# Optimization experiments

Measured on AMD Instinct MI355X. Metric: run time of the kernel, lower is better.

## Reference

```python
import jax, jax.numpy as jnp
import numpy as np

INIT_DIM = 512
HID = 1024
OUT = 64
N_NODES = 100000
N_NBR = 65536


def setup_inputs() -> dict:
    key = jax.random.key(0)
    ks = jax.random.split(key, 12)
    inp = {}
    inp["feat"] = jax.random.normal(ks[0], (1, INIT_DIM), dtype=jnp.float32)
    for i, t in enumerate("abc"):
        inp[f"all_feat_{t}"] = jax.random.normal(ks[1 + i], (N_NODES, INIT_DIM), dtype=jnp.float32)
        inp[f"nbr_{t}"] = jax.random.randint(ks[4 + i], (N_NBR,), 0, N_NODES)
        inp[f"W1_{t}"] = jax.random.normal(ks[7 + i], (HID, INIT_DIM), dtype=jnp.float32) * 0.02
        inp[f"b1_{t}"] = jnp.zeros((HID,), dtype=jnp.float32)
    inp["Wc"] = jax.random.normal(ks[10], (OUT, HID), dtype=jnp.float32) * 0.02
    inp["bc"] = jnp.zeros((OUT,), dtype=jnp.float32)
    return inp


def reference(feat, all_feat_a, all_feat_b, all_feat_c,
              nbr_a, nbr_b, nbr_c,
              W1_a, b1_a, W1_b, b1_b, W1_c, b1_c, Wc, bc):
    # trans1 = 'rel-linear': per-type neighbor gather + relation-specific Linear
    # h_j: [N_NBR, HID]
    h_a = all_feat_a[nbr_a] @ W1_a.T + b1_a
    h_b = all_feat_b[nbr_b] @ W1_b.T + b1_b
    h_c = all_feat_c[nbr_c] @ W1_c.T + b1_c
    # trans2 = 'none' (passthrough); concat aggregation over all types
    h = jnp.concatenate([h_a, h_b, h_c], axis=0)  # [3*N_NBR, HID]
    h = jax.nn.relu(h)                             # activate = 'relu'
    pooled = h.mean(axis=0)                        # agg_node = 'mean' -> [HID]
    feat_all = jax.nn.relu(pooled)
    logits = feat_all @ Wc.T + bc                  # [OUT]
    return logits
```

## Files before the change

### kernel.cpp

```cpp
#include <hip/hip_runtime.h>
#include <hip/hip_bf16.h>

typedef __attribute__((ext_vector_type(4))) float f32x4;
typedef __attribute__((ext_vector_type(4))) int   int4v;
typedef __attribute__((ext_vector_type(2))) int   int2v;
typedef __attribute__((ext_vector_type(16))) int  i32x16;

#define N_NBR 65536
#define INIT_DIM 512
#define HID 1024
#define NPAIR 1536
#define NBLOCK 256
#define PPB 6
#define SA 24.0f
#define SW 1024.0f
#define INVS (1.0f / (24.0f * 1024.0f))

static __device__ __forceinline__ int q8(float x, float s) {
  float y = fminf(fmaxf(x * s, -127.f), 127.f);
  return __float2int_rn(y);
}
static __device__ __forceinline__ int pack4(float a, float b, float c, float d, float s) {
  return (q8(a,s) & 255) | ((q8(b,s) & 255) << 8) | ((q8(c,s) & 255) << 16) | ((q8(d,s) & 255) << 24);
}

__global__ __launch_bounds__(256) void k_convw(const float* __restrict__ wa,
                                               const float* __restrict__ wb,
                                               const float* __restrict__ wc,
                                               char* __restrict__ out) {
  int g = blockIdx.x * 256 + threadIdx.x;
  int l = g & 63;
  int blk = g >> 6;
  int ks = blk & 15;
  int nb = (blk >> 4) & 31;
  int t = blk >> 9;
  const float* src = (t == 0) ? wa : (t == 1) ? wb : wc;
  int n = nb * 32 + (l & 31);
  int k0 = ks * 32 + (l >> 5) * 16;
  const f32x4* p = (const f32x4*)(src + (size_t)n * INIT_DIM + k0);
  f32x4 x0 = p[0], x1 = p[1], x2 = p[2], x3 = p[3];
  int4v v;
  v[0] = pack4(x0.x, x0.y, x0.z, x0.w, SW);
  v[1] = pack4(x1.x, x1.y, x1.z, x1.w, SW);
  v[2] = pack4(x2.x, x2.y, x2.z, x2.w, SW);
  v[3] = pack4(x3.x, x3.y, x3.z, x3.w, SW);
  *(int4v*)(out + (size_t)g * 16) = v;
}

__global__ __launch_bounds__(512, 2) void k_main(
    const float* __restrict__ fa, const float* __restrict__ fb, const float* __restrict__ fc,
    const int* __restrict__ na, const int* __restrict__ nb_, const int* __restrict__ nc__,
    const float* __restrict__ b1a, const float* __restrict__ b1b, const float* __restrict__ b1c,
    const char* __restrict__ wbf8,
    float* __restrict__ partials) {
  __shared__ __align__(16) char Asm[64 * 1024];

  int bx = blockIdx.x;
  int tid = threadIdx.x;
  int wave = tid >> 6;
  int lane = tid & 63;
  int l31 = lane & 31, hi = lane >> 5;

  unsigned swz = (unsigned)l31 << 4;
  unsigned abase = (unsigned)l31 * 1024u + (((unsigned)hi << 4) ^ (swz & 16u));
  unsigned swzhi = swz & 0x1E0u;

  for (int jp = 0; jp < PPB; ++jp) {
    int pair = bx * PPB + jp;
    int t = pair >> 9;
    int mt0 = (pair & 511) * 2;
    const float* feat = (t == 0) ? fa : (t == 1) ? fb : fc;
    const int*   nbr  = (t == 0) ? na : (t == 1) ? nb_ : nc__;
    const float* bias = (t == 0) ? b1a : (t == 1) ? b1b : b1c;
    const char*  Wf8  = wbf8 + (size_t)t * (32 * 16 * 1024);

    if (jp) __syncthreads();

    #pragma unroll
    for (int tl = 0; tl < 2; ++tl) {
      #pragma unroll 4
      for (int c = 0; c < 8; ++c) {
        int r = c * 8 + wave;
        int idx = nbr[(mt0 + tl) * 64 + r];
        const float* rp = feat + (size_t)idx * INIT_DIM + lane * 8;
        f32x4 a  = __builtin_nontemporal_load((const f32x4*)rp);
        f32x4 b2 = __builtin_nontemporal_load((const f32x4*)rp + 1);
        int2v v;
        v[0] = pack4(a.x, a.y, a.z, a.w, SA);
        v[1] = pack4(b2.x, b2.y, b2.z, b2.w, SA);
        unsigned byte = (unsigned)r * 1024u + (unsigned)(tl * 512) +
                        (((unsigned)lane * 8u) ^ ((unsigned)(r & 31) << 4));
        *(int2v*)(Asm + byte) = v;
      }
    }
    __syncthreads();

    #pragma unroll
    for (int p = 0; p < 2; ++p) {
      const char* pBa = Wf8 + ((size_t)(wave * 4 + p * 2)     << 14) + lane * 16;
      const char* pBb = Wf8 + ((size_t)(wave * 4 + p * 2 + 1) << 14) + lane * 16;

      i32x16 acc[2][2][2] = {};
      #pragma unroll 4
      for (int ks = 0; ks < 16; ++ks) {
        int4v Bf0 = *(const int4v*)(pBa + (ks << 10));
        int4v Bf1 = *(const int4v*)(pBb + (ks << 10));
        unsigned kcol = (((unsigned)ks << 5) ^ swzhi);
        int4v Af[2][2];
        #pragma unroll
        for (int tl = 0; tl < 2; ++tl)
          #pragma unroll
          for (int i = 0; i < 2; ++i)
            Af[tl][i] = *(const int4v*)(Asm + (abase + (unsigned)(tl * 512) +
                                               (unsigned)(i * 32768) + kcol));
        #pragma unroll
        for (int tl = 0; tl < 2; ++tl)
          #pragma unroll
          for (int i = 0; i < 2; ++i) {
            acc[tl][i][0] = __builtin_amdgcn_mfma_i32_32x32x32_i8(Af[tl][i], Bf0, acc[tl][i][0], 0, 0, 0);
            acc[tl][i][1] = __builtin_amdgcn_mfma_i32_32x32x32_i8(Af[tl][i], Bf1, acc[tl][i][1], 0, 0, 0);
          }
      }

      #pragma unroll
      for (int j = 0; j < 2; ++j) {
        int n = (wave * 4 + p * 2 + j) * 32 + l31;
        float b = bias[n];
        float s = 0.f;
        #pragma unroll
        for (int tl = 0; tl < 2; ++tl)
          #pragma unroll
          for (int i = 0; i < 2; ++i)
            #pragma unroll
            for (int r = 0; r < 16; ++r) {
              float v = (float)acc[tl][i][j][r] * INVS + b;
              s += fmaxf(v, 0.f);
            }
        s += __shfl_xor(s, 32);
        if (hi == 0) partials[(size_t)pair * HID + n] = s;
      }
    }
  }
}

__global__ __launch_bounds__(256) void k_reduce(const float* __restrict__ partials,
                                                float* __restrict__ acc) {
  __shared__ float red[4][64];
  int tid = threadIdx.x;
  int c = tid & 63, rg = tid >> 6;
  int col = blockIdx.x * 64 + c;
  float s = 0.f;
  #pragma unroll 4
  for (int r = rg; r < NPAIR; r += 4)
    s += partials[(size_t)r * HID + col];
  red[rg][c] = s;
  __syncthreads();
  if (rg == 0) acc[col] = red[0][c] + red[1][c] + red[2][c] + red[3][c];
}

__global__ __launch_bounds__(256) void k_final(const float* __restrict__ acc,
                                               const float* __restrict__ Wc,
                                               const float* __restrict__ bc,
                                               float* __restrict__ out) {
  __shared__ float fall[HID];
  int tid = threadIdx.x;
  const float inv = 1.f / (3.f * (float)N_NBR);
  for (int i = tid; i < HID; i += 256) {
    float p = acc[i] * inv;
    fall[i] = (p > 0.f) ? p : 0.f;
  }
  __syncthreads();
  int o = tid >> 2, q = tid & 3;
  const f32x4* w = (const f32x4*)(Wc + (size_t)o * HID + q * 256);
  const f32x4* f = (const f32x4*)(fall + q * 256);
  float s = 0.f;
  #pragma unroll 4
  for (int k = 0; k < 64; ++k) {
    f32x4 wv = w[k], fv = f[k];
    s += wv.x * fv.x + wv.y * fv.y + wv.z * fv.z + wv.w * fv.w;
  }
  s += __shfl_xor(s, 1);
  s += __shfl_xor(s, 2);
  if (q == 0) out[o] = s + bc[o];
}

extern "C" void kernel_launch(void* const* d_in, const int* in_sizes, int n_in,
                              void* d_out, int out_size, void* d_ws, size_t ws_size,
                              hipStream_t stream) {
  const float* fa  = (const float*)d_in[1];
  const int*   na  = (const int*)d_in[2];
  const float* W1a = (const float*)d_in[3];
  const float* b1a = (const float*)d_in[4];
  const float* fb  = (const float*)d_in[5];
  const int*   nb  = (const int*)d_in[6];
  const float* W1b = (const float*)d_in[7];
  const float* b1b = (const float*)d_in[8];
  const float* fc  = (const float*)d_in[9];
  const int*   nc  = (const int*)d_in[10];
  const float* W1c = (const float*)d_in[11];
  const float* b1c = (const float*)d_in[12];
  const float* Wc  = (const float*)d_in[13];
  const float* bc  = (const float*)d_in[14];
  float* out = (float*)d_out;

  float* acc = (float*)d_ws;
  char*  wbf8 = (char*)d_ws + 4096;
  float* partials = (float*)((char*)d_ws + 4096 + 3 * 32 * 16 * 1024);

  k_convw<<<384, 256, 0, stream>>>(W1a, W1b, W1c, wbf8);
  k_main<<<NBLOCK, 512, 0, stream>>>(fa, fb, fc, na, nb, nc, b1a, b1b, b1c, wbf8, partials);
  k_reduce<<<16, 256, 0, stream>>>(partials, acc);
  k_final<<<1, 256, 0, stream>>>(acc, Wc, bc, out);
}
```

Before: 212.0 us.

## Launch one 64-row tile per block and do bias+ReLU in integer domain

The persistent 256-block kernel that looped over six 128-row pairs is replaced by 3072 independent 256-thread blocks, each gathering and quantizing a single 64-row tile into 32KB of LDS. This removes the intra-block serialization between gather and MFMA phases and lets more blocks co-reside so gathers overlap with compute across blocks. The epilogue now quantizes the bias into the int32 accumulator scale and does ReLU and summation in integers, converting to float once. In exchange each block rereads its type's full weight matrix for only 64 rows, doubling weight traffic from L2, and the partials buffer and reduction grow to twice as many rows.

```diff
diff --git a/kernel.cpp b/kernel.cpp
--- a/kernel.cpp
+++ b/kernel.cpp
@@ -9,9 +9,7 @@
 #define N_NBR 65536
 #define INIT_DIM 512
 #define HID 1024
-#define NPAIR 1536
-#define NBLOCK 256
-#define PPB 6
+#define NTILE 3072
 #define SA 24.0f
 #define SW 1024.0f
 #define INVS (1.0f / (24.0f * 1024.0f))
@@ -47,98 +45,81 @@
   *(int4v*)(out + (size_t)g * 16) = v;
 }
 
-__global__ __launch_bounds__(512, 2) void k_main(
+__global__ __launch_bounds__(256) void k_main(
     const float* __restrict__ fa, const float* __restrict__ fb, const float* __restrict__ fc,
     const int* __restrict__ na, const int* __restrict__ nb_, const int* __restrict__ nc__,
     const float* __restrict__ b1a, const float* __restrict__ b1b, const float* __restrict__ b1c,
     const char* __restrict__ wbf8,
     float* __restrict__ partials) {
-  __shared__ __align__(16) char Asm[64 * 1024];
+  __shared__ __align__(16) char Asm[64 * 512];
 
   int bx = blockIdx.x;
+  int t = bx >> 10;
+  int mtile = bx & 1023;
+  const float* feat = (t == 0) ? fa : (t == 1) ? fb : fc;
+  const int*   nbr  = (t == 0) ? na : (t == 1) ? nb_ : nc__;
+  const float* bias = (t == 0) ? b1a : (t == 1) ? b1b : b1c;
+  const char*  Wf8  = wbf8 + (size_t)t * (32 * 16 * 1024);
+
   int tid = threadIdx.x;
   int wave = tid >> 6;
   int lane = tid & 63;
   int l31 = lane & 31, hi = lane >> 5;
 
+  #pragma unroll 4
+  for (int c = 0; c < 16; ++c) {
+    int r = c * 4 + wave;
+    int idx = nbr[mtile * 64 + r];
+    const float* rp = feat + (size_t)idx * INIT_DIM + lane * 8;
+    f32x4 a  = __builtin_nontemporal_load((const f32x4*)rp);
+    f32x4 b2 = __builtin_nontemporal_load((const f32x4*)rp + 1);
+    int2v v;
+    v[0] = pack4(a.x, a.y, a.z, a.w, SA);
+    v[1] = pack4(b2.x, b2.y, b2.z, b2.w, SA);
+    unsigned byte = (unsigned)r * 512u +
+                    (((unsigned)lane * 8u) ^ ((unsigned)(r & 31) << 4));
+    *(int2v*)(Asm + byte) = v;
+  }
+  __syncthreads();
+
   unsigned swz = (unsigned)l31 << 4;
-  unsigned abase = (unsigned)l31 * 1024u + (((unsigned)hi << 4) ^ (swz & 16u));
+  unsigned abase = (unsigned)l31 * 512u + (((unsigned)hi << 4) ^ (swz & 16u));
   unsigned swzhi = swz & 0x1E0u;
 
-  for (int jp = 0; jp < PPB; ++jp) {
-    int pair = bx * PPB + jp;
-    int t = pair >> 9;
-    int mt0 = (pair & 511) * 2;
-    const float* feat = (t == 0) ? fa : (t == 1) ? fb : fc;
-    const int*   nbr  = (t == 0) ? na : (t == 1) ? nb_ : nc__;
-    const float* bias = (t == 0) ? b1a : (t == 1) ? b1b : b1c;
-    const char*  Wf8  = wbf8 + (size_t)t * (32 * 16 * 1024);
+  #pragma unroll
+  for (int p = 0; p < 4; ++p) {
+    const char* pBa = Wf8 + ((size_t)(wave * 8 + p * 2)     << 14) + lane * 16;
+    const char* pBb = Wf8 + ((size_t)(wave * 8 + p * 2 + 1) << 14) + lane * 16;
 
-    if (jp) __syncthreads();
+    i32x16 acc[2][2] = {};
+    #pragma unroll 4
+    for (int ks = 0; ks < 16; ++ks) {
+      int4v Bf0 = *(const int4v*)(pBa + (ks << 10));
+      int4v Bf1 = *(const int4v*)(pBb + (ks << 10));
+      unsigned kcol = (((unsigned)ks << 5) ^ swzhi);
+      int4v Af[2];
+      #pragma unroll
+      for (int i = 0; i < 2; ++i)
+        Af[i] = *(const int4v*)(Asm + (abase + (unsigned)(i * 16384) + kcol));
+      #pragma unroll
+      for (int i = 0; i < 2; ++i) {
+        acc[i][0] = __builtin_amdgcn_mfma_i32_32x32x32_i8(Af[i], Bf0, acc[i][0], 0, 0, 0);
+        acc[i][1] = __builtin_amdgcn_mfma_i32_32x32x32_i8(Af[i], Bf1, acc[i][1], 0, 0, 0);
+      }
+    }
 
     #pragma unroll
-    for (int tl = 0; tl < 2; ++tl) {
-      #pragma unroll 4
-      for (int c = 0; c < 8; ++c) {
-        int r = c * 8 + wave;
-        int idx = nbr[(mt0 + tl) * 64 + r];
-        const float* rp = feat + (size_t)idx * INIT_DIM + lane * 8;
-        f32x4 a  = __builtin_nontemporal_load((const f32x4*)rp);
-        f32x4 b2 = __builtin_nontemporal_load((const f32x4*)rp + 1);
-        int2v v;
-        v[0] = pack4(a.x, a.y, a.z, a.w, SA);
-        v[1] = pack4(b2.x, b2.y, b2.z, b2.w, SA);
-        unsigned byte = (unsigned)r * 1024u + (unsigned)(tl * 512) +
-                        (((unsigned)lane * 8u) ^ ((unsigned)(r & 31) << 4));
-        *(int2v*)(Asm + byte) = v;
-      }
-    }
-    __syncthreads();
-
-    #pragma unroll
-    for (int p = 0; p < 2; ++p) {
-      const char* pBa = Wf8 + ((size_t)(wave * 4 + p * 2)     << 14) + lane * 16;
-      const char* pBb = Wf8 + ((size_t)(wave * 4 + p * 2 + 1) << 14) + lane * 16;
-
-      i32x16 acc[2][2][2] = {};
-      #pragma unroll 4
-      for (int ks = 0; ks < 16; ++ks) {
-        int4v Bf0 = *(const int4v*)(pBa + (ks << 10));
-        int4v Bf1 = *(const int4v*)(pBb + (ks << 10));
-        unsigned kcol = (((unsigned)ks << 5) ^ swzhi);
-        int4v Af[2][2];
+    for (int j = 0; j < 2; ++j) {
+      int n = (wave * 8 + p * 2 + j) * 32 + l31;
+      int bq = __float2int_rn(bias[n] * (SA * SW));
+      int s = 0;
+      #pragma unroll
+      for (int i = 0; i < 2; ++i)
         #pragma unroll
-        for (int tl = 0; tl < 2; ++tl)
-          #pragma unroll
-          for (int i = 0; i < 2; ++i)
-            Af[tl][i] = *(const int4v*)(Asm + (abase + (unsigned)(tl * 512) +
-                                               (unsigned)(i * 32768) + kcol));
-        #pragma unroll
-        for (int tl = 0; tl < 2; ++tl)
-          #pragma unroll
-          for (int i = 0; i < 2; ++i) {
-            acc[tl][i][0] = __builtin_amdgcn_mfma_i32_32x32x32_i8(Af[tl][i], Bf0, acc[tl][i][0], 0, 0, 0);
-            acc[tl][i][1] = __builtin_amdgcn_mfma_i32_32x32x32_i8(Af[tl][i], Bf1, acc[tl][i][1], 0, 0, 0);
-          }
-      }
-
-      #pragma unroll
-      for (int j = 0; j < 2; ++j) {
-        int n = (wave * 4 + p * 2 + j) * 32 + l31;
-        float b = bias[n];
-        float s = 0.f;
-        #pragma unroll
-        for (int tl = 0; tl < 2; ++tl)
-          #pragma unroll
-          for (int i = 0; i < 2; ++i)
-            #pragma unroll
-            for (int r = 0; r < 16; ++r) {
-              float v = (float)acc[tl][i][j][r] * INVS + b;
-              s += fmaxf(v, 0.f);
-            }
-        s += __shfl_xor(s, 32);
-        if (hi == 0) partials[(size_t)pair * HID + n] = s;
-      }
+        for (int r = 0; r < 16; ++r)
+          s += max(acc[i][j][r] + bq, 0);
+      s += __shfl_xor(s, 32);
+      if (hi == 0) partials[(size_t)bx * HID + n] = (float)s * INVS;
     }
   }
 }
@@ -151,7 +132,7 @@
   int col = blockIdx.x * 64 + c;
   float s = 0.f;
   #pragma unroll 4
-  for (int r = rg; r < NPAIR; r += 4)
+  for (int r = rg; r < NTILE; r += 4)
     s += partials[(size_t)r * HID + col];
   red[rg][c] = s;
   __syncthreads();
@@ -208,7 +189,7 @@
   float* partials = (float*)((char*)d_ws + 4096 + 3 * 32 * 16 * 1024);
 
   k_convw<<<384, 256, 0, stream>>>(W1a, W1b, W1c, wbf8);
-  k_main<<<NBLOCK, 512, 0, stream>>>(fa, fb, fc, na, nb, nc, b1a, b1b, b1c, wbf8, partials);
+  k_main<<<NTILE, 256, 0, stream>>>(fa, fb, fc, na, nb, nc, b1a, b1b, b1c, wbf8, partials);
   k_reduce<<<16, 256, 0, stream>>>(partials, acc);
   k_final<<<1, 256, 0, stream>>>(acc, Wc, bc, out);
 }
```

New measurement: 240.7 us. 13.5% more time.
